# Optimization experiments

Hardware: AMD Instinct MI355X
Metric: run time of the kernel (lower is better)

## Reference

```python
import jax, jax.numpy as jnp
import numpy as np

B, T, D = 64, 512, 204
H1, H2, FC, OUT = 512, 256, 512, 7


def _lstm_layer(x, Wih, Whh, bih, bhh):
    """PyTorch-style LSTM (gate order i,f,g,o), batch_first. x: [B,T,D] -> [B,T,H]."""
    b = x.shape[0]
    h_dim = Whh.shape[1]
    # One big GEMM for the input projection across all timesteps.
    xg = jnp.einsum('btd,gd->btg', x, Wih) + bih + bhh  # [B,T,4H]

    def step(carry, xt):
        h, c = carry
        g = xt + h @ Whh.T  # [B,4H]
        i, f, gg, o = jnp.split(g, 4, axis=-1)
        i = jax.nn.sigmoid(i)
        f = jax.nn.sigmoid(f)
        gg = jnp.tanh(gg)
        o = jax.nn.sigmoid(o)
        c = f * c + i * gg
        h = o * jnp.tanh(c)
        return (h, c), h

    h0 = jnp.zeros((b, h_dim), x.dtype)
    (_, _), hs = jax.lax.scan(step, (h0, h0), jnp.swapaxes(xg, 0, 1))  # hs: [T,B,H]
    return jnp.swapaxes(hs, 0, 1)


def setup_inputs() -> dict:
    key = jax.random.key(0)
    ks = jax.random.split(key, 14)
    s1 = 1.0 / np.sqrt(H1)
    s2 = 1.0 / np.sqrt(H2)
    sf = 1.0 / np.sqrt(FC)
    return {
        'x': jax.random.normal(ks[0], (B, T, D), jnp.float32),
        'W_ih1': jax.random.uniform(ks[1], (4 * H1, D), jnp.float32, -s1, s1),
        'W_hh1': jax.random.uniform(ks[2], (4 * H1, H1), jnp.float32, -s1, s1),
        'b_ih1': jax.random.uniform(ks[3], (4 * H1,), jnp.float32, -s1, s1),
        'b_hh1': jax.random.uniform(ks[4], (4 * H1,), jnp.float32, -s1, s1),
        'W_ih2': jax.random.uniform(ks[5], (4 * H2, H1), jnp.float32, -s2, s2),
        'W_hh2': jax.random.uniform(ks[6], (4 * H2, H2), jnp.float32, -s2, s2),
        'b_ih2': jax.random.uniform(ks[7], (4 * H2,), jnp.float32, -s2, s2),
        'b_hh2': jax.random.uniform(ks[8], (4 * H2,), jnp.float32, -s2, s2),
        'W_fc1': jax.random.uniform(ks[9], (FC, H2), jnp.float32, -s2, s2),
        'b_fc1': jax.random.uniform(ks[10], (FC,), jnp.float32, -s2, s2),
        'W_fc2': jax.random.uniform(ks[11], (OUT, FC), jnp.float32, -sf, sf),
        'b_fc2': jax.random.uniform(ks[12], (OUT,), jnp.float32, -sf, sf),
    }


def reference(x, W_ih1, W_hh1, b_ih1, b_hh1, W_ih2, W_hh2, b_ih2, b_hh2,
              W_fc1, b_fc1, W_fc2, b_fc2):
    h1 = _lstm_layer(x, W_ih1, W_hh1, b_ih1, b_hh1)    # [B,T,H1]
    h2 = _lstm_layer(h1, W_ih2, W_hh2, b_ih2, b_hh2)   # [B,T,H2]
    last = h2[:, -1, :]                                 # [B,H2]
    z = jax.nn.relu(last @ W_fc1.T + b_fc1)             # [B,FC]
    return z @ W_fc2.T + b_fc2                          # [B,OUT]
```

## Files before the change

### kernel.cpp

```cpp
#include <hip/hip_runtime.h>

#define TT   512
#define BB   64
#define HH1  512
#define HH2  256
#define DD   204
#define L1B  64
#define L2B  32
#define NBLK (L1B+L2B)
#define FCN  512

typedef _Float16 half8 __attribute__((ext_vector_type(8)));
typedef float    f32x4 __attribute__((ext_vector_type(4)));

__device__ __align__(16) float g_xg[TT][L1B][32][BB];
__device__ __align__(16) _Float16 g_h1[TT+1][HH1/8][BB][8];
__device__ __align__(16) _Float16 g_h2[TT+1][HH2/8][BB][8];
__device__ float g_z[BB][FCN];
struct __align__(128) Flag { unsigned v; unsigned pad[31]; };
__device__ Flag g_flag1[L1B];
__device__ Flag g_flag2[L2B];
__device__ unsigned g_ctr0;

__device__ __forceinline__ float sigm(float x){ return 1.0f/(1.0f + __expf(-x)); }
__device__ __forceinline__ float tanha(float x){ return 1.0f - 2.0f/(__expf(2.0f*x) + 1.0f); }

__device__ __forceinline__ void awrite(unsigned* p, unsigned v){
  __hip_atomic_store(p, v, __ATOMIC_RELAXED, __HIP_MEMORY_SCOPE_AGENT);
}
__device__ __forceinline__ void awrite64(unsigned long long* p, unsigned long long v){
  __hip_atomic_store(p, v, __ATOMIC_RELAXED, __HIP_MEMORY_SCOPE_AGENT);
}
__device__ __forceinline__ unsigned aread(unsigned* p){
  return __hip_atomic_load(p, __ATOMIC_RELAXED, __HIP_MEMORY_SCOPE_AGENT);
}
__device__ __forceinline__ void wait_ge(unsigned* c, unsigned target){
  while (aread(c) < target) __builtin_amdgcn_s_sleep(8);
  asm volatile("" ::: "memory");
}
__device__ __forceinline__ unsigned short h16(_Float16 h){
  union { _Float16 f; unsigned short u; } cv; cv.f = h; return cv.u;
}

#define MFMA16 __builtin_amdgcn_mfma_f32_16x16x32_f16

__global__ __launch_bounds__(256) void k_xg(const float* __restrict__ x,
                                            const float* __restrict__ Wih1){
  __shared__ __align__(16) _Float16 sAh[28][64][8];
  __shared__ __align__(16) _Float16 sAl[28][64][8];
  const int tid = threadIdx.x;
  const int blk = blockIdx.x & 31, tc = blockIdx.x >> 5;
  const int l = tid & 63, w = tid >> 6, n = l & 15, kq = l >> 4;

  half8 Bh[7], Bl[7];
  {
    int grow = (n>>2)*HH1 + blk*16 + (w>>1)*8 + (w&1)*4 + (n&3);
    #pragma unroll
    for (int ks = 0; ks < 7; ++ks){
      int k0 = ks*32 + kq*8;
      half8 hi, lo;
      #pragma unroll
      for (int jj = 0; jj < 8; ++jj){
        float v = (k0 + jj < DD) ? Wih1[grow*DD + k0 + jj] : 0.f;
        _Float16 h = (_Float16)v;
        hi[jj] = h; lo[jj] = (_Float16)(v - (float)h);
      }
      Bh[ks] = hi; Bl[ks] = lo;
    }
  }

  for (int t = tc*64; t < tc*64 + 64; ++t){
    __syncthreads();
    for (int idx = tid; idx < 64*28; idx += 256){
      int b = idx & 63, ko = idx >> 6;
      int d0 = ko*8;
      const float* xp = &x[(b*TT + t)*DD];
      float4 va = (d0 + 3 < DD) ? *(const float4*)&xp[d0]     : float4{0,0,0,0};
      float4 vb = (d0 + 7 < DD) ? *(const float4*)&xp[d0 + 4] : float4{0,0,0,0};
      float vv[8] = {va.x,va.y,va.z,va.w, vb.x,vb.y,vb.z,vb.w};
      half8 hi, lo;
      #pragma unroll
      for (int jj = 0; jj < 8; ++jj){
        _Float16 h = (_Float16)vv[jj];
        hi[jj] = h; lo[jj] = (_Float16)(vv[jj] - (float)h);
      }
      *(half8*)&sAh[ko][b][0] = hi;
      *(half8*)&sAl[ko][b][0] = lo;
    }
    __syncthreads();
    #pragma unroll
    for (int mt = 0; mt < 4; ++mt){
      f32x4 a0 = {0,0,0,0}, a1 = a0, a2 = a0;
      #pragma unroll
      for (int ks = 0; ks < 7; ++ks){
        half8 ah = *(const half8*)&sAh[ks*4 + kq][mt*16 + n][0];
        half8 al = *(const half8*)&sAl[ks*4 + kq][mt*16 + n][0];
        a0 = MFMA16(ah, Bh[ks], a0, 0,0,0);
        a1 = MFMA16(ah, Bl[ks], a1, 0,0,0);
        a2 = MFMA16(al, Bh[ks], a2, 0,0,0);
      }
      f32x4 v4;
      v4[0] = (a0[0] + a1[0]) + a2[0];
      v4[1] = (a0[1] + a1[1]) + a2[1];
      v4[2] = (a0[2] + a1[2]) + a2[2];
      v4[3] = (a0[3] + a1[3]) + a2[3];
      __builtin_nontemporal_store(v4, (f32x4*)&g_xg[t][blk*2 + (w>>1)][(w&1)*16 + n][mt*16 + kq*4]);
    }
  }
}

#define LOADA(AH, KB, SH) {                                 \
  _Pragma("unroll")                                         \
  for (int j = 0; j < 4; ++j)                               \
    AH[j] = SH[(((KB)+j)*4 + kq)*BB + mrow];                \
  }
#define COMPC1(AH, KB) {                                    \
  _Pragma("unroll")                                         \
  for (int j = 0; j < 4; ++j)                               \
    p0 = MFMA16(AH[j], Bh[(KB)+j], p0, 0,0,0);              \
  }

__global__ __launch_bounds__(512, 2) void k_scan(
    const float* Whh1, const float* bih1, const float* bhh1,
    const float* Wih2, const float* Whh2,
    const float* bih2, const float* bhh2)
{
  const int bid = blockIdx.x;
  const int tid = threadIdx.x;
  const int l  = tid & 63;
  const int w  = tid >> 6;
  const int n  = l & 15;
  const int kq = l >> 4;
  const int ug = w >> 2;
  const int mt = w & 3;
  const int mrow = mt*16 + n;
  const int mout = mt*16 + kq*4;

  {
    int eidx = bid*512 + tid;
    unsigned* z1 = (unsigned*)&g_h1[0][0][0][0];
    if (eidx < (HH1*BB)/2) awrite(z1 + eidx, 0u);
    unsigned* z2 = (unsigned*)&g_h2[0][0][0][0];
    if (eidx < (HH2*BB)/2) awrite(z2 + eidx, 0u);
  }

  if (bid < L1B){
    const int b1 = bid;
    half8 Bh[16];
    {
      const float* wr = &Whh1[((size_t)((n>>2)*HH1 + b1*8 + ug*4 + (n&3)))*HH1];
      #pragma unroll
      for (int ks = 0; ks < 16; ++ks){
        float4 a = *(const float4*)&wr[ks*32 + kq*8];
        float4 b = *(const float4*)&wr[ks*32 + kq*8 + 4];
        float vv[8] = {a.x,a.y,a.z,a.w, b.x,b.y,b.z,b.w};
        half8 hi;
        #pragma unroll
        for (int j = 0; j < 8; ++j) hi[j] = (_Float16)vv[j];
        Bh[ks] = hi;
      }
    }
    float bias;
    {
      int gi = (n>>2)*HH1 + b1*8 + ug*4 + (n&3);
      bias = bih1[gi] + bhh1[gi];
    }
    asm volatile("s_waitcnt vmcnt(0)" ::: "memory");
    __syncthreads();
    if (tid == 0){
      __hip_atomic_fetch_add(&g_ctr0, 1u, __ATOMIC_RELAXED, __HIP_MEMORY_SCOPE_AGENT);
      wait_ge(&g_ctr0, NBLK);
    }
    __syncthreads();

    float cst[4] = {0,0,0,0};
    for (int t = 0; t < TT; ++t){
      f32x4 xgv = __builtin_nontemporal_load((const f32x4*)&g_xg[t][b1][ug*16 + n][mout]);
      if (w == 0 && t > 0){
        unsigned* f = &g_flag1[l].v;
        while (!__all(aread(f) >= (unsigned)t)) __builtin_amdgcn_s_sleep(2);
      }
      __syncthreads();

      const half8* Ah = (const half8*)&g_h1[t][0][0][0];
      f32x4 p0 = {0,0,0,0};
      half8 a0[4], a1[4], a2[4], a3[4];
      LOADA(a0, 0,  Ah);
      LOADA(a1, 4,  Ah);
      LOADA(a2, 8,  Ah);
      LOADA(a3, 12, Ah);
      COMPC1(a0, 0);
      COMPC1(a1, 4);
      COMPC1(a2, 8);
      COMPC1(a3, 12);

      #pragma unroll
      for (int r = 0; r < 4; ++r){
        float v = p0[r] + bias + xgv[r];
        float act = (n >= 8 && n < 12) ? tanha(v) : sigm(v);
        float fx = __shfl_xor(act, 4);
        float gx = __shfl_xor(act, 8);
        float cn = fx*cst[r] + act*gx;
        float tc = tanha(cn);
        if (n < 4) cst[r] = cn;
        float tcx = __shfl_xor(tc, 12);
        float hv = act * tcx;
        float hx = __shfl_xor(hv, 1);
        unsigned hw = (unsigned)h16((_Float16)hv) | ((unsigned)h16((_Float16)hx) << 16);
        unsigned hw2 = __shfl_xor(hw, 2);
        if (n == 12){
          int m = mout + r;
          unsigned long long v64 = (unsigned long long)hw | ((unsigned long long)hw2 << 32);
          awrite64((unsigned long long*)((unsigned*)&g_h1[t+1][b1][m][0] + ug*2), v64);
        }
      }
      asm volatile("s_waitcnt vmcnt(0)" ::: "memory");
      __syncthreads();
      if (tid == 0) awrite(&g_flag1[b1].v, (unsigned)(t + 1));
    }
  } else {
    const int b2 = bid - L1B;
    half8 Bh[24];
    {
      int grow = (n>>2)*HH2 + b2*8 + ug*4 + (n&3);
      const float* w1 = &Wih2[(size_t)grow*HH1];
      #pragma unroll
      for (int ks = 0; ks < 16; ++ks){
        float4 a = *(const float4*)&w1[ks*32 + kq*8];
        float4 b = *(const float4*)&w1[ks*32 + kq*8 + 4];
        float vv[8] = {a.x,a.y,a.z,a.w, b.x,b.y,b.z,b.w};
        half8 hi;
        #pragma unroll
        for (int j = 0; j < 8; ++j) hi[j] = (_Float16)vv[j];
        Bh[ks] = hi;
      }
      const float* w2 = &Whh2[(size_t)grow*HH2];
      #pragma unroll
      for (int ks = 0; ks < 8; ++ks){
        float4 a = *(const float4*)&w2[ks*32 + kq*8];
        float4 b = *(const float4*)&w2[ks*32 + kq*8 + 4];
        float vv[8] = {a.x,a.y,a.z,a.w, b.x,b.y,b.z,b.w};
        half8 hi;
        #pragma unroll
        for (int j = 0; j < 8; ++j) hi[j] = (_Float16)vv[j];
        Bh[16 + ks] = hi;
      }
    }
    float bias;
    {
      int gi = (n>>2)*HH2 + b2*8 + ug*4 + (n&3);
      bias = bih2[gi] + bhh2[gi];
    }
    asm volatile("s_waitcnt vmcnt(0)" ::: "memory");
    __syncthreads();
    if (tid == 0){
      __hip_atomic_fetch_add(&g_ctr0, 1u, __ATOMIC_RELAXED, __HIP_MEMORY_SCOPE_AGENT);
      wait_ge(&g_ctr0, NBLK);
    }
    __syncthreads();

    float cst[4] = {0,0,0,0};
    for (int t = 0; t < TT; ++t){
      if (w == 0){
        unsigned* f1 = &g_flag1[l].v;
        unsigned* f2 = &g_flag2[l & 31].v;
        while (true){
          unsigned a = aread(f1);
          unsigned b = aread(f2);
          if (__all(a >= (unsigned)(t + 1) && b >= (unsigned)t)) break;
          __builtin_amdgcn_s_sleep(2);
        }
      }
      __syncthreads();

      const half8* Ah = (const half8*)&g_h1[t+1][0][0][0];
      const half8* Ch = (const half8*)&g_h2[t][0][0][0];
      f32x4 p0 = {0,0,0,0};
      half8 a0[4], a1[4], a2[4];
      LOADA(a0, 0, Ah);
      LOADA(a1, 4, Ah);
      LOADA(a2, 8, Ah);
      COMPC1(a0, 0);   LOADA(a0, 12, Ah);
      COMPC1(a1, 4);   LOADA(a1, 0,  Ch);
      COMPC1(a2, 8);   LOADA(a2, 4,  Ch);
      COMPC1(a0, 12);
      COMPC1(a1, 16);
      COMPC1(a2, 20);

      #pragma unroll
      for (int r = 0; r < 4; ++r){
        float v = p0[r] + bias;
        float act = (n >= 8 && n < 12) ? tanha(v) : sigm(v);
        float fx = __shfl_xor(act, 4);
        float gx = __shfl_xor(act, 8);
        float cn = fx*cst[r] + act*gx;
        float tc = tanha(cn);
        if (n < 4) cst[r] = cn;
        float tcx = __shfl_xor(tc, 12);
        float hv = act * tcx;
        float hx = __shfl_xor(hv, 1);
        unsigned hw = (unsigned)h16((_Float16)hv) | ((unsigned)h16((_Float16)hx) << 16);
        unsigned hw2 = __shfl_xor(hw, 2);
        if (n == 12){
          int m = mout + r;
          unsigned long long v64 = (unsigned long long)hw | ((unsigned long long)hw2 << 32);
          awrite64((unsigned long long*)((unsigned*)&g_h2[t+1][b2][m][0] + ug*2), v64);
        }
      }
      asm volatile("s_waitcnt vmcnt(0)" ::: "memory");
      __syncthreads();
      if (tid == 0) awrite(&g_flag2[b2].v, (unsigned)(t + 1));
    }
  }
}

__global__ __launch_bounds__(256) void k_fc1(const float* __restrict__ Wfc1, const float* __restrict__ bfc1){
  int b = blockIdx.x;
  for (int task = threadIdx.x; task < 512; task += 256){
    int m = task >> 3, cc = b*8 + (task & 7);
    float acc = bfc1[cc];
    const float* wr = &Wfc1[cc*HH2];
    for (int k = 0; k < HH2; ++k){
      float hvv = (float)g_h2[TT][k>>3][m][k&7];
      acc += hvv * wr[k];
    }
    g_z[m][cc] = fmaxf(acc, 0.f);
  }
}

__global__ __launch_bounds__(256) void k_fc2(const float* __restrict__ Wfc2, const float* __restrict__ bfc2,
                                             float* __restrict__ out){
  for (int task = threadIdx.x; task < BB*7; task += 256){
    int m = task / 7, oc = task % 7;
    float acc = bfc2[oc];
    const float* wr = &Wfc2[oc*FCN];
    const float* zr = &g_z[m][0];
    for (int k = 0; k < FCN; ++k) acc += zr[k]*wr[k];
    out[m*7 + oc] = acc;
  }
  if (threadIdx.x < L1B) awrite(&g_flag1[threadIdx.x].v, 0u);
  if (threadIdx.x < L2B) awrite(&g_flag2[threadIdx.x].v, 0u);
  if (threadIdx.x == 0)  awrite(&g_ctr0, 0u);
}

extern "C" void kernel_launch(void* const* d_in, const int* in_sizes, int n_in,
                              void* d_out, int out_size, void* d_ws, size_t ws_size,
                              hipStream_t stream){
  (void)in_sizes; (void)n_in; (void)out_size; (void)d_ws; (void)ws_size;
  const float* x    = (const float*)d_in[0];
  const float* Wih1 = (const float*)d_in[1];
  const float* Whh1 = (const float*)d_in[2];
  const float* bih1 = (const float*)d_in[3];
  const float* bhh1 = (const float*)d_in[4];
  const float* Wih2 = (const float*)d_in[5];
  const float* Whh2 = (const float*)d_in[6];
  const float* bih2 = (const float*)d_in[7];
  const float* bhh2 = (const float*)d_in[8];
  const float* Wfc1 = (const float*)d_in[9];
  const float* bfc1 = (const float*)d_in[10];
  const float* Wfc2 = (const float*)d_in[11];
  const float* bfc2 = (const float*)d_in[12];

  hipLaunchKernelGGL(k_xg,   dim3(256), dim3(256), 0, stream, x, Wih1);
  hipLaunchKernelGGL(k_scan, dim3(NBLK), dim3(512), 0, stream,
                     Whh1, bih1, bhh1, Wih2, Whh2, bih2, bhh2);
  hipLaunchKernelGGL(k_fc1,  dim3(FCN/8), dim3(256), 0, stream, Wfc1, bfc1);
  hipLaunchKernelGGL(k_fc2,  dim3(1), dim3(256), 0, stream, Wfc2, bfc2, (float*)d_out);
}
```

Baseline: 2.753 ms.

## Halve layer-1 block count with two hidden-unit slices per warp; split layer-2 wait

```diff
diff --git a/kernel.cpp b/kernel.cpp
--- a/kernel.cpp
+++ b/kernel.cpp
@@ -5,7 +5,7 @@
 #define HH1  512
 #define HH2  256
 #define DD   204
-#define L1B  64
+#define L1B  32
 #define L2B  32
 #define NBLK (L1B+L2B)
 #define FCN  512
@@ -13,7 +13,7 @@
 typedef _Float16 half8 __attribute__((ext_vector_type(8)));
 typedef float    f32x4 __attribute__((ext_vector_type(4)));
 
-__device__ __align__(16) float g_xg[TT][L1B][32][BB];
+__device__ __align__(16) float g_xg[TT][64][32][BB];
 __device__ __align__(16) _Float16 g_h1[TT+1][HH1/8][BB][8];
 __device__ __align__(16) _Float16 g_h2[TT+1][HH2/8][BB][8];
 __device__ float g_z[BB][FCN];
@@ -119,6 +119,12 @@
   for (int j = 0; j < 4; ++j)                               \
     p0 = MFMA16(AH[j], Bh[(KB)+j], p0, 0,0,0);              \
   }
+#define COMP2Q(AH, KB) {                                    \
+  _Pragma("unroll")                                         \
+  for (int j = 0; j < 4; ++j){                              \
+    p0 = MFMA16(AH[j], Bh0[(KB)+j], p0, 0,0,0);             \
+    p1 = MFMA16(AH[j], Bh1[(KB)+j], p1, 0,0,0);             \
+  } }
 
 __global__ __launch_bounds__(512, 2) void k_scan(
     const float* Whh1, const float* bih1, const float* bhh1,
@@ -131,7 +137,6 @@
   const int w  = tid >> 6;
   const int n  = l & 15;
   const int kq = l >> 4;
-  const int ug = w >> 2;
   const int mt = w & 3;
   const int mrow = mt*16 + n;
   const int mout = mt*16 + kq*4;
@@ -146,9 +151,13 @@
 
   if (bid < L1B){
     const int b1 = bid;
-    half8 Bh[16];
-    {
-      const float* wr = &Whh1[((size_t)((n>>2)*HH1 + b1*8 + ug*4 + (n&3)))*HH1];
+    const int ug2 = w >> 2;
+    half8 Bh0[16], Bh1[16];
+    float bias0, bias1;
+    #pragma unroll
+    for (int q = 0; q < 2; ++q){
+      int grow = (n>>2)*HH1 + b1*16 + (ug2*2 + q)*4 + (n&3);
+      const float* wr = &Whh1[(size_t)grow*HH1];
       #pragma unroll
       for (int ks = 0; ks < 16; ++ks){
         float4 a = *(const float4*)&wr[ks*32 + kq*8];
@@ -157,13 +166,10 @@
         half8 hi;
         #pragma unroll
         for (int j = 0; j < 8; ++j) hi[j] = (_Float16)vv[j];
-        Bh[ks] = hi;
-      }
-    }
-    float bias;
-    {
-      int gi = (n>>2)*HH1 + b1*8 + ug*4 + (n&3);
-      bias = bih1[gi] + bhh1[gi];
+        if (q == 0) Bh0[ks] = hi; else Bh1[ks] = hi;
+      }
+      float bv = bih1[grow] + bhh1[grow];
+      if (q == 0) bias0 = bv; else bias1 = bv;
     }
     asm volatile("s_waitcnt vmcnt(0)" ::: "memory");
     __syncthreads();
@@ -173,18 +179,120 @@
     }
     __syncthreads();
 
+    float cst[2][4] = {{0,0,0,0},{0,0,0,0}};
+    for (int t = 0; t < TT; ++t){
+      f32x4 xg0 = __builtin_nontemporal_load((const f32x4*)&g_xg[t][2*b1 + ug2][n][mout]);
+      f32x4 xg1 = __builtin_nontemporal_load((const f32x4*)&g_xg[t][2*b1 + ug2][16 + n][mout]);
+      if (w == 0 && t > 0){
+        unsigned* f = &g_flag1[l & 31].v;
+        while (!__all(aread(f) >= (unsigned)t)) __builtin_amdgcn_s_sleep(2);
+      }
+      __syncthreads();
+
+      const half8* Ah = (const half8*)&g_h1[t][0][0][0];
+      f32x4 p0 = {0,0,0,0}, p1 = p0;
+      half8 a0[4], a1[4], a2[4], a3[4];
+      LOADA(a0, 0,  Ah);
+      LOADA(a1, 4,  Ah);
+      LOADA(a2, 8,  Ah);
+      LOADA(a3, 12, Ah);
+      COMP2Q(a0, 0);
+      COMP2Q(a1, 4);
+      COMP2Q(a2, 8);
+      COMP2Q(a3, 12);
+
+      #pragma unroll
+      for (int q = 0; q < 2; ++q){
+        #pragma unroll
+        for (int r = 0; r < 4; ++r){
+          float v = (q ? p1[r] : p0[r]) + (q ? bias1 : bias0) + (q ? xg1[r] : xg0[r]);
+          float act = (n >= 8 && n < 12) ? tanha(v) : sigm(v);
+          float fx = __shfl_xor(act, 4);
+          float gx = __shfl_xor(act, 8);
+          float cn = fx*cst[q][r] + act*gx;
+          float tc = tanha(cn);
+          if (n < 4) cst[q][r] = cn;
+          float tcx = __shfl_xor(tc, 12);
+          float hv = act * tcx;
+          float hx = __shfl_xor(hv, 1);
+          unsigned hw = (unsigned)h16((_Float16)hv) | ((unsigned)h16((_Float16)hx) << 16);
+          unsigned hw2 = __shfl_xor(hw, 2);
+          if (n == 12){
+            int m = mout + r;
+            unsigned long long v64 = (unsigned long long)hw | ((unsigned long long)hw2 << 32);
+            awrite64((unsigned long long*)((unsigned*)&g_h1[t+1][2*b1 + ug2][m][0] + q*2), v64);
+          }
+        }
+      }
+      asm volatile("s_waitcnt vmcnt(0)" ::: "memory");
+      __syncthreads();
+      if (tid == 0) awrite(&g_flag1[b1].v, (unsigned)(t + 1));
+    }
+  } else {
+    const int b2 = bid - L1B;
+    const int ug = w >> 2;
+    half8 Bh[24];
+    {
+      int grow = (n>>2)*HH2 + b2*8 + ug*4 + (n&3);
+      const float* w1 = &Wih2[(size_t)grow*HH1];
+      #pragma unroll
+      for (int ks = 0; ks < 16; ++ks){
+        float4 a = *(const float4*)&w1[ks*32 + kq*8];
+        float4 b = *(const float4*)&w1[ks*32 + kq*8 + 4];
+        float vv[8] = {a.x,a.y,a.z,a.w, b.x,b.y,b.z,b.w};
+        half8 hi;
+        #pragma unroll
+        for (int j = 0; j < 8; ++j) hi[j] = (_Float16)vv[j];
+        Bh[ks] = hi;
+      }
+      const float* w2 = &Whh2[(size_t)grow*HH2];
+      #pragma unroll
+      for (int ks = 0; ks < 8; ++ks){
+        float4 a = *(const float4*)&w2[ks*32 + kq*8];
+        float4 b = *(const float4*)&w2[ks*32 + kq*8 + 4];
+        float vv[8] = {a.x,a.y,a.z,a.w, b.x,b.y,b.z,b.w};
+        half8 hi;
+        #pragma unroll
+        for (int j = 0; j < 8; ++j) hi[j] = (_Float16)vv[j];
+        Bh[16 + ks] = hi;
+      }
+    }
+    float bias;
+    {
+      int gi = (n>>2)*HH2 + b2*8 + ug*4 + (n&3);
+      bias = bih2[gi] + bhh2[gi];
+    }
+    asm volatile("s_waitcnt vmcnt(0)" ::: "memory");
+    __syncthreads();
+    if (tid == 0){
+      __hip_atomic_fetch_add(&g_ctr0, 1u, __ATOMIC_RELAXED, __HIP_MEMORY_SCOPE_AGENT);
+      wait_ge(&g_ctr0, NBLK);
+    }
+    __syncthreads();
+
     float cst[4] = {0,0,0,0};
     for (int t = 0; t < TT; ++t){
-      f32x4 xgv = __builtin_nontemporal_load((const f32x4*)&g_xg[t][b1][ug*16 + n][mout]);
       if (w == 0 && t > 0){
-        unsigned* f = &g_flag1[l].v;
-        while (!__all(aread(f) >= (unsigned)t)) __builtin_amdgcn_s_sleep(2);
-      }
-      __syncthreads();
-
-      const half8* Ah = (const half8*)&g_h1[t][0][0][0];
+        unsigned* f2 = &g_flag2[l & 31].v;
+        while (!__all(aread(f2) >= (unsigned)t)) __builtin_amdgcn_s_sleep(2);
+      }
+      __syncthreads();
+
+      const half8* Ch = (const half8*)&g_h2[t][0][0][0];
       f32x4 p0 = {0,0,0,0};
       half8 a0[4], a1[4], a2[4], a3[4];
+      LOADA(a0, 0, Ch);
+      LOADA(a1, 4, Ch);
+      COMPC1(a0, 16);
+      COMPC1(a1, 20);
+
+      if (w == 0){
+        unsigned* f1 = &g_flag1[l & 31].v;
+        while (!__all(aread(f1) >= (unsigned)(t + 1))) __builtin_amdgcn_s_sleep(2);
+      }
+      __syncthreads();
+
+      const half8* Ah = (const half8*)&g_h1[t+1][0][0][0];
       LOADA(a0, 0,  Ah);
       LOADA(a1, 4,  Ah);
       LOADA(a2, 8,  Ah);
@@ -193,99 +301,6 @@
       COMPC1(a1, 4);
       COMPC1(a2, 8);
       COMPC1(a3, 12);
-
-      #pragma unroll
-      for (int r = 0; r < 4; ++r){
-        float v = p0[r] + bias + xgv[r];
-        float act = (n >= 8 && n < 12) ? tanha(v) : sigm(v);
-        float fx = __shfl_xor(act, 4);
-        float gx = __shfl_xor(act, 8);
-        float cn = fx*cst[r] + act*gx;
-        float tc = tanha(cn);
-        if (n < 4) cst[r] = cn;
-        float tcx = __shfl_xor(tc, 12);
-        float hv = act * tcx;
-        float hx = __shfl_xor(hv, 1);
-        unsigned hw = (unsigned)h16((_Float16)hv) | ((unsigned)h16((_Float16)hx) << 16);
-        unsigned hw2 = __shfl_xor(hw, 2);
-        if (n == 12){
-          int m = mout + r;
-          unsigned long long v64 = (unsigned long long)hw | ((unsigned long long)hw2 << 32);
-          awrite64((unsigned long long*)((unsigned*)&g_h1[t+1][b1][m][0] + ug*2), v64);
-        }
-      }
-      asm volatile("s_waitcnt vmcnt(0)" ::: "memory");
-      __syncthreads();
-      if (tid == 0) awrite(&g_flag1[b1].v, (unsigned)(t + 1));
-    }
-  } else {
-    const int b2 = bid - L1B;
-    half8 Bh[24];
-    {
-      int grow = (n>>2)*HH2 + b2*8 + ug*4 + (n&3);
-      const float* w1 = &Wih2[(size_t)grow*HH1];
-      #pragma unroll
-      for (int ks = 0; ks < 16; ++ks){
-        float4 a = *(const float4*)&w1[ks*32 + kq*8];
-        float4 b = *(const float4*)&w1[ks*32 + kq*8 + 4];
-        float vv[8] = {a.x,a.y,a.z,a.w, b.x,b.y,b.z,b.w};
-        half8 hi;
-        #pragma unroll
-        for (int j = 0; j < 8; ++j) hi[j] = (_Float16)vv[j];
-        Bh[ks] = hi;
-      }
-      const float* w2 = &Whh2[(size_t)grow*HH2];
-      #pragma unroll
-      for (int ks = 0; ks < 8; ++ks){
-        float4 a = *(const float4*)&w2[ks*32 + kq*8];
-        float4 b = *(const float4*)&w2[ks*32 + kq*8 + 4];
-        float vv[8] = {a.x,a.y,a.z,a.w, b.x,b.y,b.z,b.w};
-        half8 hi;
-        #pragma unroll
-        for (int j = 0; j < 8; ++j) hi[j] = (_Float16)vv[j];
-        Bh[16 + ks] = hi;
-      }
-    }
-    float bias;
-    {
-      int gi = (n>>2)*HH2 + b2*8 + ug*4 + (n&3);
-      bias = bih2[gi] + bhh2[gi];
-    }
-    asm volatile("s_waitcnt vmcnt(0)" ::: "memory");
-    __syncthreads();
-    if (tid == 0){
-      __hip_atomic_fetch_add(&g_ctr0, 1u, __ATOMIC_RELAXED, __HIP_MEMORY_SCOPE_AGENT);
-      wait_ge(&g_ctr0, NBLK);
-    }
-    __syncthreads();
-
-    float cst[4] = {0,0,0,0};
-    for (int t = 0; t < TT; ++t){
-      if (w == 0){
-        unsigned* f1 = &g_flag1[l].v;
-        unsigned* f2 = &g_flag2[l & 31].v;
-        while (true){
-          unsigned a = aread(f1);
-          unsigned b = aread(f2);
-          if (__all(a >= (unsigned)(t + 1) && b >= (unsigned)t)) break;
-          __builtin_amdgcn_s_sleep(2);
-        }
-      }
-      __syncthreads();
-
-      const half8* Ah = (const half8*)&g_h1[t+1][0][0][0];
-      const half8* Ch = (const half8*)&g_h2[t][0][0][0];
-      f32x4 p0 = {0,0,0,0};
-      half8 a0[4], a1[4], a2[4];
-      LOADA(a0, 0, Ah);
-      LOADA(a1, 4, Ah);
-      LOADA(a2, 8, Ah);
-      COMPC1(a0, 0);   LOADA(a0, 12, Ah);
-      COMPC1(a1, 4);   LOADA(a1, 0,  Ch);
-      COMPC1(a2, 8);   LOADA(a2, 4,  Ch);
-      COMPC1(a0, 12);
-      COMPC1(a1, 16);
-      COMPC1(a2, 20);
 
       #pragma unroll
       for (int r = 0; r < 4; ++r){
```

Result: slower. 2.893 ms (+5.1%).
